# Optimization experiments

Hardware: AMD Instinct MI355X
Metric: run time of the kernel (lower is better)

## Reference

```python
import jax, jax.numpy as jnp
import numpy as np

N = 50000      # nodes
E = 1600000    # message edges (avg degree 32)
EQ = 500000    # link-prediction query edges
IN, HID, OUT, FCH = 128, 128, 64, 256
ALPHA = 0.5


def setup_inputs() -> dict:
    key = jax.random.key(0)
    ks = jax.random.split(key, 8)
    def p(k, shape):
        fan_in = shape[0]
        return jax.random.normal(k, shape, jnp.float32) * (1.0 / np.sqrt(fan_in))
    return {
        "x": jax.random.normal(ks[0], (N, IN), jnp.float32),
        "edge_index": jax.random.randint(ks[1], (2, E), 0, N),
        "edge_label_index": jax.random.randint(ks[2], (2, EQ), 0, N),
        "W1": p(ks[3], (IN, HID)),  "b1": jnp.zeros((HID,), jnp.float32),
        "W2": p(ks[4], (HID, OUT)), "b2": jnp.zeros((OUT,), jnp.float32),
        "Wf1": p(ks[5], (IN, FCH)), "bf1": jnp.zeros((FCH,), jnp.float32),
        "Wf2": p(ks[6], (FCH, OUT)), "bf2": jnp.zeros((OUT,), jnp.float32),
    }


def reference(x, edge_index, edge_label_index, W1, b1, W2, b2, Wf1, bf1, Wf2, bf2):
    n = x.shape[0]
    # GCN self-loops + symmetric normalization (PyG GCNConv defaults)
    loop = jnp.arange(n)
    src = jnp.concatenate([edge_index[0], loop])
    dst = jnp.concatenate([edge_index[1], loop])
    deg = jax.ops.segment_sum(jnp.ones_like(dst, jnp.float32), dst, num_segments=n)
    dinv = jnp.where(deg > 0, jax.lax.rsqrt(deg), 0.0)
    norm = dinv[src] * dinv[dst]  # [E+N]

    def gcn(h, W, b):
        h = h @ W                                  # transform first (PyG order)
        msg = norm[:, None] * h[src]               # gather + scale per edge
        return jax.ops.segment_sum(msg, dst, num_segments=n) + b

    x_gcn = jax.nn.relu(gcn(x, W1, b1))
    x_gcn = gcn(x_gcn, W2, b2)
    x_fc = jax.nn.relu(x @ Wf1 + bf1) @ Wf2 + bf2
    z = x_gcn * (1.0 - ALPHA) + x_fc * ALPHA       # [N, OUT]
    # edge dot-product decode
    return jnp.sum(z[edge_label_index[0]] * z[edge_label_index[1]], axis=1)
```

## Files before the change

### kernel.cpp

```cpp
#include <hip/hip_runtime.h>

#define FIN   128
#define FHID  128
#define FOUT  64
#define FFC   256
#define CHUNK 4096
#define BKBITS 7
#define BKN   128
#define ECAP  4608

typedef __attribute__((ext_vector_type(8))) short          bf16x8;
typedef __attribute__((ext_vector_type(4))) float          f32x4;
typedef __attribute__((ext_vector_type(2))) float          f32x2;
typedef __attribute__((ext_vector_type(8))) unsigned short u16x8;

static __device__ __forceinline__ unsigned short f2bf(float f) {
    unsigned int u = __float_as_uint(f);
    u = (u + 0x7fffu + ((u >> 16) & 1u)) >> 16;
    return (unsigned short)u;
}
static __device__ __forceinline__ float bf2f(unsigned short s) {
    return __uint_as_float(((unsigned int)s) << 16);
}
static __device__ __forceinline__ void accum_fp8(float* acc, uint4 g) {
    f32x2 p;
    p = __builtin_amdgcn_cvt_pk_f32_fp8(g.x, false); acc[0]  += p.x; acc[1]  += p.y;
    p = __builtin_amdgcn_cvt_pk_f32_fp8(g.x, true);  acc[2]  += p.x; acc[3]  += p.y;
    p = __builtin_amdgcn_cvt_pk_f32_fp8(g.y, false); acc[4]  += p.x; acc[5]  += p.y;
    p = __builtin_amdgcn_cvt_pk_f32_fp8(g.y, true);  acc[6]  += p.x; acc[7]  += p.y;
    p = __builtin_amdgcn_cvt_pk_f32_fp8(g.z, false); acc[8]  += p.x; acc[9]  += p.y;
    p = __builtin_amdgcn_cvt_pk_f32_fp8(g.z, true);  acc[10] += p.x; acc[11] += p.y;
    p = __builtin_amdgcn_cvt_pk_f32_fp8(g.w, false); acc[12] += p.x; acc[13] += p.y;
    p = __builtin_amdgcn_cvt_pk_f32_fp8(g.w, true);  acc[14] += p.x; acc[15] += p.y;
}

__global__ __launch_bounds__(256) void cvt_kernel(
    const float* __restrict__ W1, const float* __restrict__ W2,
    const float* __restrict__ Wf1, const float* __restrict__ Wf2,
    unsigned short* __restrict__ w1t, unsigned short* __restrict__ w2t,
    unsigned short* __restrict__ wf1t, unsigned short* __restrict__ wf2t)
{
    long i = (long)blockIdx.x * 256 + threadIdx.x;
    if (i < 16384) {
        int k = (int)i >> 7, n = (int)i & 127;
        w1t[n * 128 + k] = f2bf(W1[i]);
    } else if (i < 24576) {
        int j = (int)i - 16384; int k = j >> 6, n = j & 63;
        w2t[n * 128 + k] = f2bf(W2[j]);
    } else if (i < 57344) {
        int j = (int)i - 24576; int k = j >> 8, n = j & 255;
        wf1t[n * 128 + k] = f2bf(Wf1[j]);
    } else if (i < 73728) {
        int j = (int)i - 57344; int k = j >> 6, n = j & 63;
        wf2t[n * 256 + k] = f2bf(Wf2[j]);
    }
}

__global__ __launch_bounds__(256) void binA_fc_kernel(
    const int* __restrict__ src, const int* __restrict__ dst,
    int* __restrict__ bcur, unsigned int* __restrict__ ebuf, int E, int NBA,
    const float* __restrict__ X,
    const unsigned short* __restrict__ B1T,
    const unsigned short* __restrict__ B2T,
    const float* __restrict__ bias1, const float* __restrict__ bias2,
    unsigned short* __restrict__ C, int M)
{
    __shared__ __align__(16) unsigned char smem[49152];
    const int tid = threadIdx.x;

    if (blockIdx.x < NBA) {
        int* hist   = (int*)smem;
        int* rstart = (int*)(smem + 2048);
        int* lcur   = (int*)(smem + 4096);
        int t = tid;
        hist[t] = 0; hist[t + 256] = 0; lcur[t] = 0; lcur[t + 256] = 0;
        __syncthreads();
        int e0 = blockIdx.x * CHUNK;
        int cnt_e = min(CHUNK, E - e0);
        int sreg[16], dreg[16];
        #pragma unroll
        for (int i = 0; i < 16; i++) {
            int o = t + i * 256;
            bool ok = o < cnt_e;
            sreg[i] = ok ? src[e0 + o] : 0;
            dreg[i] = ok ? dst[e0 + o] : 0;
            if (ok) ;
        }
        #pragma unroll
        for (int i = 0; i < 16; i++)
            if (t + i * 256 < cnt_e) atomicAdd(&hist[dreg[i] >> BKBITS], 1);
        __syncthreads();
        if (hist[t])       rstart[t]       = atomicAdd(&bcur[t],       hist[t]);
        if (hist[t + 256]) rstart[t + 256] = atomicAdd(&bcur[t + 256], hist[t + 256]);
        __syncthreads();
        #pragma unroll
        for (int i = 0; i < 16; i++) {
            if (t + i * 256 < cnt_e) {
                int s = sreg[i], d = dreg[i];
                int b = d >> BKBITS;
                int pos = rstart[b] + atomicAdd(&lcur[b], 1);
                if (pos < ECAP)
                    ebuf[(size_t)b * ECAP + pos] =
                        ((unsigned)s << BKBITS) | ((unsigned)d & (BKN - 1));
            }
        }
        return;
    }

    unsigned short* lds = (unsigned short*)smem;
    const int lane = tid & 63;
    const int wave = tid >> 6;
    const int m = lane & 15;
    const int q = lane >> 4;
    const int rowbase = (blockIdx.x - NBA) * 64 + wave * 16;
    const int row = rowbase + m;

    float4 av[8] = {};
    {
        const float* arow = X + (size_t)row * FIN + q * 8;
        if (row < M) {
            #pragma unroll
            for (int kk = 0; kk < 4; kk++) {
                av[2 * kk]     = *(const float4*)(arow + kk * 32);
                av[2 * kk + 1] = *(const float4*)(arow + kk * 32 + 4);
            }
        }
    }

    #pragma unroll 2
    for (int i = tid; i < 2048; i += 256) {
        int n = i >> 4, sl = i & 15;
        ((u16x8*)lds)[(n << 4) | (sl ^ (n & 7))] = ((const u16x8*)B1T)[i];
    }
    __syncthreads();

    f32x4 acc[16] = {};
    for (int k0 = 0; k0 < 128; k0 += 32) {
        int kk = k0 >> 5;
        float4 a0 = av[2 * kk], a1 = av[2 * kk + 1];
        bf16x8 a;
        a[0] = (short)f2bf(a0.x); a[1] = (short)f2bf(a0.y);
        a[2] = (short)f2bf(a0.z); a[3] = (short)f2bf(a0.w);
        a[4] = (short)f2bf(a1.x); a[5] = (short)f2bf(a1.y);
        a[6] = (short)f2bf(a1.z); a[7] = (short)f2bf(a1.w);
        int sl = q + (k0 >> 3);
        #pragma unroll
        for (int c = 0; c < 8; c++) {
            int cc = c * 16 + m;
            bf16x8 b = ((const bf16x8*)lds)[(cc << 4) | (sl ^ (cc & 7))];
            acc[c] = __builtin_amdgcn_mfma_f32_16x16x32_bf16(a, b, acc[c], 0, 0, 0);
        }
    }
    __syncthreads();
    #pragma unroll 2
    for (int i = tid; i < 2048; i += 256) {
        int n = i >> 4, sl = i & 15;
        ((u16x8*)lds)[(n << 4) | (sl ^ (n & 7))] = ((const u16x8*)B1T)[2048 + i];
    }
    __syncthreads();
    for (int k0 = 0; k0 < 128; k0 += 32) {
        int kk = k0 >> 5;
        float4 a0 = av[2 * kk], a1 = av[2 * kk + 1];
        bf16x8 a;
        a[0] = (short)f2bf(a0.x); a[1] = (short)f2bf(a0.y);
        a[2] = (short)f2bf(a0.z); a[3] = (short)f2bf(a0.w);
        a[4] = (short)f2bf(a1.x); a[5] = (short)f2bf(a1.y);
        a[6] = (short)f2bf(a1.z); a[7] = (short)f2bf(a1.w);
        int sl = q + (k0 >> 3);
        #pragma unroll
        for (int c = 0; c < 8; c++) {
            int cc = c * 16 + m;
            bf16x8 b = ((const bf16x8*)lds)[(cc << 4) | (sl ^ (cc & 7))];
            acc[8 + c] = __builtin_amdgcn_mfma_f32_16x16x32_bf16(a, b, acc[8 + c], 0, 0, 0);
        }
    }
    __syncthreads();
    #pragma unroll
    for (int c = 0; c < 16; c++) {
        int cc = c * 16 + m;
        float bv = bias1[cc];
        #pragma unroll
        for (int r = 0; r < 4; r++) {
            int rr = wave * 16 + q * 4 + r;
            float v = fmaxf(acc[c][r] + bv, 0.f);
            lds[rr * 256 + ((((cc >> 3) ^ (rr & 7)) << 3) | (cc & 7))] = f2bf(v);
        }
    }
    for (int i = tid; i < 1024; i += 256) {
        int n = i >> 4, sl = i & 15;
        ((u16x8*)lds)[2048 + ((n << 4) | (sl ^ (n & 7)))] =
            ((const u16x8*)B2T)[n * 32 + sl];
    }
    __syncthreads();

    f32x4 acc2[4] = {};
    {
        int rr = wave * 16 + m;
        for (int k0 = 0; k0 < 128; k0 += 32) {
            int sl = q + (k0 >> 3);
            bf16x8 a = ((const bf16x8*)lds)[(rr << 5) | (sl ^ (rr & 7))];
            #pragma unroll
            for (int c = 0; c < 4; c++) {
                int cc = c * 16 + m;
                bf16x8 b = ((const bf16x8*)lds)[2048 + ((cc << 4) | (sl ^ (cc & 7)))];
                acc2[c] = __builtin_amdgcn_mfma_f32_16x16x32_bf16(a, b, acc2[c], 0, 0, 0);
            }
        }
    }
    __syncthreads();
    for (int i = tid; i < 1024; i += 256) {
        int n = i >> 4, sl = i & 15;
        ((u16x8*)lds)[2048 + ((n << 4) | (sl ^ (n & 7)))] =
            ((const u16x8*)B2T)[n * 32 + 16 + sl];
    }
    __syncthreads();
    {
        int rr = wave * 16 + m;
        for (int k0 = 128; k0 < 256; k0 += 32) {
            int sla = q + (k0 >> 3);
            int slb = q + ((k0 - 128) >> 3);
            bf16x8 a = ((const bf16x8*)lds)[(rr << 5) | (sla ^ (rr & 7))];
            #pragma unroll
            for (int c = 0; c < 4; c++) {
                int cc = c * 16 + m;
                bf16x8 b = ((const bf16x8*)lds)[2048 + ((cc << 4) | (slb ^ (cc & 7)))];
                acc2[c] = __builtin_amdgcn_mfma_f32_16x16x32_bf16(a, b, acc2[c], 0, 0, 0);
            }
        }
    }
    __syncthreads();

    constexpr int ROWB = 4 * 16 * 2 + 16;
    unsigned char* wbase = (unsigned char*)lds + wave * 16 * ROWB;
    #pragma unroll
    for (int c = 0; c < 4; c++) {
        int lc = c * 16 + m;
        float bv = bias2[lc];
        #pragma unroll
        for (int r = 0; r < 4; r++)
            ((unsigned short*)(wbase + (q * 4 + r) * ROWB))[lc] =
                f2bf(acc2[c][r] + bv);
    }
    #pragma unroll
    for (int p = 0; p < 2; p++) {
        int r2 = p * 8 + (lane >> 3);
        int bo = (lane & 7) * 16;
        int gr = rowbase + r2;
        if (gr < M) {
            uint4 v = *(const uint4*)(wbase + r2 * ROWB + bo);
            *(uint4*)((unsigned char*)C + (size_t)gr * FOUT * 2 + bo) = v;
        }
    }
}

__global__ __launch_bounds__(256) void binB_kernel(
    const unsigned int* __restrict__ ebuf, const int* __restrict__ bcnt,
    int2* __restrict__ rp2, int* __restrict__ col, float* __restrict__ dinv,
    const float* __restrict__ x, unsigned char* __restrict__ xs, int N)
{
    __shared__ __align__(16) unsigned char smem[40448];
    int* cnt           = (int*)smem;
    int* tmp           = (int*)(smem + 512);
    int* ccur          = (int*)(smem + 1536);
    int* scur          = (int*)(smem + 2048);
    float* sdinv       = (float*)(smem + 3072);
    unsigned int* skey = (unsigned int*)(smem + 3584);
    int* colLds        = (int*)(smem + 22016);
    int b = blockIdx.x;
    int t = threadIdx.x;
    size_t base = (size_t)b * ECAP;
    int ne = min(bcnt[b], ECAP);
    if (t < 128) cnt[t] = 0;
    scur[t] = 0;
    __syncthreads();
    for (int e = t; e < ne; e += 256) {
        unsigned int k = ebuf[base + e];
        atomicAdd(&cnt[k & (BKN - 1)], 1);
        atomicAdd(&scur[k >> 15], 1);
    }
    __syncthreads();
    int c = (t < 128) ? cnt[t] : 0;
    tmp[t] = c;
    __syncthreads();
    int acc = c;
    for (int off = 1; off < 128; off <<= 1) {
        int a = (t >= off) ? tmp[t - off] : 0;
        __syncthreads();
        acc += a; tmp[t] = acc;
        __syncthreads();
    }
    if (t < 128) {
        float di = rsqrtf((float)c + 1.0f);
        sdinv[t] = di;
        int node = b * BKN + t;
        int st = (int)base + acc - c;
        if (node < N) { dinv[node] = di; rp2[node] = make_int2(st, st + c); }
        ccur[t] = acc - c;
    }
    __syncthreads();
    int sv = scur[t];
    tmp[t] = sv;
    __syncthreads();
    int sacc = sv;
    for (int off = 1; off < 256; off <<= 1) {
        int a = (t >= off) ? tmp[t - off] : 0;
        __syncthreads();
        sacc += a; tmp[t] = sacc;
        __syncthreads();
    }
    scur[t] = sacc - sv;
    __syncthreads();
    for (int e = t; e < ne; e += 256) {
        unsigned int k = ebuf[base + e];
        int pos = atomicAdd(&scur[k >> 15], 1);
        skey[pos] = k;
    }
    __syncthreads();
    for (int w = 0; w < ne; w += 256) {
        int e = w + t;
        if (e < ne) {
            unsigned int k = skey[e];
            int pos = atomicAdd(&ccur[k & (BKN - 1)], 1);
            colLds[pos] = (int)(k >> BKBITS);
        }
        __syncthreads();
    }
    for (int e = t; e < ne; e += 256)
        col[base + e] = colLds[e];
    int nl0 = t >> 3;
    int f0 = (t & 7) << 4;
    #pragma unroll
    for (int it = 0; it < 4; it++) {
        int nl = it * 32 + nl0;
        int gn = b * BKN + nl;
        if (gn >= N) continue;
        float d2 = sdinv[nl];
        const float* xr = x + (size_t)gn * FIN + f0;
        float4 va = *(const float4*)(xr);
        float4 vb = *(const float4*)(xr + 4);
        float4 vc = *(const float4*)(xr + 8);
        float4 vd = *(const float4*)(xr + 12);
        float f[16] = { va.x * d2, va.y * d2, va.z * d2, va.w * d2,
                        vb.x * d2, vb.y * d2, vb.z * d2, vb.w * d2,
                        vc.x * d2, vc.y * d2, vc.z * d2, vc.w * d2,
                        vd.x * d2, vd.y * d2, vd.z * d2, vd.w * d2 };
        uint4 w;
        w.x = 0; w.y = 0; w.z = 0; w.w = 0;
        w.x = __builtin_amdgcn_cvt_pk_fp8_f32(f[0],  f[1],  w.x, false);
        w.x = __builtin_amdgcn_cvt_pk_fp8_f32(f[2],  f[3],  w.x, true);
        w.y = __builtin_amdgcn_cvt_pk_fp8_f32(f[4],  f[5],  w.y, false);
        w.y = __builtin_amdgcn_cvt_pk_fp8_f32(f[6],  f[7],  w.y, true);
        w.z = __builtin_amdgcn_cvt_pk_fp8_f32(f[8],  f[9],  w.z, false);
        w.z = __builtin_amdgcn_cvt_pk_fp8_f32(f[10], f[11], w.z, true);
        w.w = __builtin_amdgcn_cvt_pk_fp8_f32(f[12], f[13], w.w, false);
        w.w = __builtin_amdgcn_cvt_pk_fp8_f32(f[14], f[15], w.w, true);
        *(uint4*)(xs + (size_t)gn * 128 + f0) = w;
    }
}

__global__ __launch_bounds__(256) void pull1_kernel(
    const unsigned char* __restrict__ xs, const int2* __restrict__ rp2,
    const int* __restrict__ col, const float* __restrict__ dinv,
    unsigned short* __restrict__ aggx, int N)
{
    int tid = threadIdx.x;
    int node = blockIdx.x * 32 + (tid >> 3);
    if (node >= N) return;
    int f0 = (tid & 7) << 4;
    const unsigned char* base = xs + f0;
    float di = dinv[node];
    int2 se = rp2[node];
    float acc[16] = {};
    accum_fp8(acc, *(const uint4*)(base + (size_t)node * 128));
    int e = se.x, end = se.y;
    for (; e + 4 <= end; e += 4) {
        int s0 = col[e], s1 = col[e + 1], s2 = col[e + 2], s3 = col[e + 3];
        uint4 g0 = *(const uint4*)(base + (size_t)s0 * 128);
        uint4 g1 = *(const uint4*)(base + (size_t)s1 * 128);
        uint4 g2 = *(const uint4*)(base + (size_t)s2 * 128);
        uint4 g3 = *(const uint4*)(base + (size_t)s3 * 128);
        accum_fp8(acc, g0); accum_fp8(acc, g1);
        accum_fp8(acc, g2); accum_fp8(acc, g3);
    }
    for (; e < end; e++)
        accum_fp8(acc, *(const uint4*)(base + (size_t)col[e] * 128));
    u16x8 o0, o1;
    #pragma unroll
    for (int j = 0; j < 8; j++) {
        o0[j] = f2bf(di * acc[j]);
        o1[j] = f2bf(di * acc[8 + j]);
    }
    *(u16x8*)(aggx + (size_t)node * FIN + f0)     = o0;
    *(u16x8*)(aggx + (size_t)node * FIN + f0 + 8) = o1;
}

__global__ __launch_bounds__(256) void gcn_kernel(
    const unsigned short* __restrict__ A,
    const unsigned short* __restrict__ B1T,
    const unsigned short* __restrict__ B2T,
    const float* __restrict__ bias1,
    const float* __restrict__ rowscale,
    unsigned short* __restrict__ C, int M)
{
    __shared__ __align__(16) unsigned short lds[16384];
    const int tid  = threadIdx.x;
    const int lane = tid & 63;
    const int wave = tid >> 6;
    const int m = lane & 15;
    const int q = lane >> 4;
    const int rowbase = blockIdx.x * 64 + wave * 16;
    const int row = rowbase + m;

    bf16x8 areg[4] = {};
    {
        const unsigned short* arow = A + (size_t)row * FIN + q * 8;
        if (row < M) {
            #pragma unroll
            for (int kk = 0; kk < 4; kk++)
                areg[kk] = *(const bf16x8*)(arow + kk * 32);
        }
    }

    #pragma unroll 2
    for (int i = tid; i < 2048; i += 256) {
        int n = i >> 4, sl = i & 15;
        ((u16x8*)lds)[(n << 4) | (sl ^ (n & 7))] = ((const u16x8*)B1T)[i];
    }
    __syncthreads();

    f32x4 acc[8] = {};
    for (int k0 = 0; k0 < 128; k0 += 32) {
        bf16x8 a = areg[k0 >> 5];
        int sl = q + (k0 >> 3);
        #pragma unroll
        for (int c = 0; c < 8; c++) {
            int cc = c * 16 + m;
            bf16x8 b = ((const bf16x8*)lds)[(cc << 4) | (sl ^ (cc & 7))];
            acc[c] = __builtin_amdgcn_mfma_f32_16x16x32_bf16(a, b, acc[c], 0, 0, 0);
        }
    }
    __syncthreads();

    #pragma unroll
    for (int c = 0; c < 8; c++) {
        int cc = c * 16 + m;
        float bv = bias1[cc];
        #pragma unroll
        for (int r = 0; r < 4; r++) {
            int rr = wave * 16 + q * 4 + r;
            float v = fmaxf(acc[c][r] + bv, 0.f);
            lds[rr * 128 + ((((cc >> 3) ^ (rr & 7)) << 3) | (cc & 7))] = f2bf(v);
        }
    }
    for (int i = tid; i < 1024; i += 256) {
        int n = i >> 4, sl = i & 15;
        ((u16x8*)lds)[1024 + ((n << 4) | (sl ^ (n & 7)))] = ((const u16x8*)B2T)[i];
    }
    __syncthreads();

    f32x4 acc2[4] = {};
    {
        int rr = wave * 16 + m;
        for (int k0 = 0; k0 < 128; k0 += 32) {
            int sl = q + (k0 >> 3);
            bf16x8 a = ((const bf16x8*)lds)[(rr << 4) | (sl ^ (rr & 7))];
            #pragma unroll
            for (int c = 0; c < 4; c++) {
                int cc = c * 16 + m;
                bf16x8 b = ((const bf16x8*)lds)[1024 + ((cc << 4) | (sl ^ (cc & 7)))];
                acc2[c] = __builtin_amdgcn_mfma_f32_16x16x32_bf16(a, b, acc2[c], 0, 0, 0);
            }
        }
    }
    float rs[4];
    #pragma unroll
    for (int r = 0; r < 4; r++) {
        int gr = rowbase + q * 4 + r;
        rs[r] = (gr < M) ? rowscale[gr] : 1.0f;
    }
    __syncthreads();

    constexpr int ROWB = 4 * 16 * 2 + 16;
    unsigned char* wbase = (unsigned char*)lds + wave * 16 * ROWB;
    #pragma unroll
    for (int c = 0; c < 4; c++) {
        int lc = c * 16 + m;
        #pragma unroll
        for (int r = 0; r < 4; r++)
            ((unsigned short*)(wbase + (q * 4 + r) * ROWB))[lc] =
                f2bf(acc2[c][r] * rs[r]);
    }
    #pragma unroll
    for (int p = 0; p < 2; p++) {
        int r2 = p * 8 + (lane >> 3);
        int bo = (lane & 7) * 16;
        int gr = rowbase + r2;
        if (gr < M) {
            uint4 v = *(const uint4*)(wbase + r2 * ROWB + bo);
            *(uint4*)((unsigned char*)C + (size_t)gr * FOUT * 2 + bo) = v;
        }
    }
}

__global__ __launch_bounds__(256) void pull2_kernel(
    const unsigned short* __restrict__ t2s, const int2* __restrict__ rp2,
    const int* __restrict__ col, const float* __restrict__ dinv,
    const unsigned short* __restrict__ xfc, const float* __restrict__ b2,
    unsigned short* __restrict__ zbf, int N)
{
    int tid = threadIdx.x;
    int node = blockIdx.x * 32 + (tid >> 3);
    if (node >= N) return;
    int f0 = (tid & 7) << 3;
    const unsigned short* base = t2s + f0;
    float di = dinv[node];
    u16x8 xv = *(const u16x8*)(xfc + (size_t)node * FOUT + f0);
    float4 bb0 = *(const float4*)(b2 + f0);
    float4 bb1 = *(const float4*)(b2 + f0 + 4);
    u16x8 own = *(const u16x8*)(base + (size_t)node * FOUT);
    float acc[8];
    #pragma unroll
    for (int j = 0; j < 8; j++) acc[j] = bf2f(own[j]);
    int2 se = rp2[node];
    int e = se.x, end = se.y;
    for (; e + 4 <= end; e += 4) {
        int s0 = col[e], s1 = col[e + 1], s2 = col[e + 2], s3 = col[e + 3];
        u16x8 v0 = *(const u16x8*)(base + (size_t)s0 * FOUT);
        u16x8 v1 = *(const u16x8*)(base + (size_t)s1 * FOUT);
        u16x8 v2 = *(const u16x8*)(base + (size_t)s2 * FOUT);
        u16x8 v3 = *(const u16x8*)(base + (size_t)s3 * FOUT);
        #pragma unroll
        for (int j = 0; j < 8; j++)
            acc[j] += (bf2f(v0[j]) + bf2f(v1[j])) + (bf2f(v2[j]) + bf2f(v3[j]));
    }
    for (; e < end; e++) {
        u16x8 v = *(const u16x8*)(base + (size_t)col[e] * FOUT);
        #pragma unroll
        for (int j = 0; j < 8; j++) acc[j] += bf2f(v[j]);
    }
    float bv[8] = { bb0.x, bb0.y, bb0.z, bb0.w, bb1.x, bb1.y, bb1.z, bb1.w };
    u16x8 o;
    #pragma unroll
    for (int j = 0; j < 8; j++)
        o[j] = f2bf(0.5f * (di * acc[j] + bv[j]) + 0.5f * bf2f(xv[j]));
    *(u16x8*)(zbf + (size_t)node * FOUT + f0) = o;
}

__global__ void decode_kernel(
    const unsigned short* __restrict__ zbf, const int* __restrict__ eli,
    float* __restrict__ out, int Q)
{
    int tid = blockIdx.x * blockDim.x + threadIdx.x;
    int q = tid >> 3;
    if (q >= Q) return;
    int lane = tid & 7;
    int a = eli[q];
    int b = eli[Q + q];
    u16x8 va = *(const u16x8*)(zbf + (size_t)a * FOUT + lane * 8);
    u16x8 vb = *(const u16x8*)(zbf + (size_t)b * FOUT + lane * 8);
    float s = 0.f;
    #pragma unroll
    for (int j = 0; j < 8; j++) s += bf2f(va[j]) * bf2f(vb[j]);
    s += __shfl_down(s, 4, 8);
    s += __shfl_down(s, 2, 8);
    s += __shfl_down(s, 1, 8);
    if (lane == 0) out[q] = s;
}

extern "C" void kernel_launch(void* const* d_in, const int* in_sizes, int n_in,
                              void* d_out, int out_size, void* d_ws, size_t ws_size,
                              hipStream_t stream)
{
    const float* x   = (const float*)d_in[0];
    const int*   ei  = (const int*)  d_in[1];
    const int*   eli = (const int*)  d_in[2];
    const float* W1  = (const float*)d_in[3];
    const float* b1  = (const float*)d_in[4];
    const float* W2  = (const float*)d_in[5];
    const float* b2  = (const float*)d_in[6];
    const float* Wf1 = (const float*)d_in[7];
    const float* bf1 = (const float*)d_in[8];
    const float* Wf2 = (const float*)d_in[9];
    const float* bf2 = (const float*)d_in[10];
    float* out = (float*)d_out;

    const int N = in_sizes[0] / FIN;
    const int E = in_sizes[1] / 2;
    const int Q = in_sizes[2] / 2;
    const int* src = ei;
    const int* dst = ei + E;
    const int NBK = (N + BKN - 1) >> BKBITS;
    const int NBA = (E + CHUNK - 1) / CHUNK;
    const int NCV = 73728 / 256;
    const int NFC = (N + 63) / 64;

    char* p = (char*)d_ws;
    float* dinv = (float*)p;             p += (size_t)N * 4;
    int2*  rp2  = (int2*)p;              p += (size_t)N * 8;
    int*   bcur = (int*)p;               p += 2048;
    unsigned short* w1t  = (unsigned short*)p; p += FIN * FHID * 2;
    unsigned short* w2t  = (unsigned short*)p; p += FHID * FOUT * 2;
    unsigned short* wf1t = (unsigned short*)p; p += FIN * FFC * 2;
    unsigned short* wf2t = (unsigned short*)p; p += FFC * FOUT * 2;
    unsigned short* xfc = (unsigned short*)p;  p += (size_t)N * FOUT * 2;
    unsigned char* xs = (unsigned char*)p;     p += (size_t)N * 128;
    unsigned int* ebuf = (unsigned int*)p;  p += (size_t)NBK * ECAP * 4;
    int*   col  = (int*)p;               p += (size_t)NBK * ECAP * 4;
    unsigned short* aggx = (unsigned short*)p; p += (size_t)N * FIN * 2;
    unsigned short* t2s  = (unsigned short*)p; p += (size_t)N * FOUT * 2;
    unsigned short* zbf  = (unsigned short*)p; p += (size_t)N * FOUT * 2;

    const int TB = 256;

    hipMemsetAsync(bcur, 0, 2048, stream);

    cvt_kernel<<<NCV, TB, 0, stream>>>(
        W1, W2, Wf1, Wf2, w1t, w2t, wf1t, wf2t);

    binA_fc_kernel<<<NBA + NFC, TB, 0, stream>>>(
        src, dst, bcur, ebuf, E, NBA,
        x, wf1t, wf2t, bf1, bf2, xfc, N);

    binB_kernel<<<NBK, TB, 0, stream>>>(ebuf, bcur, rp2, col, dinv, x, xs, N);

    pull1_kernel<<<(N + 31) / 32, TB, 0, stream>>>(xs, rp2, col, dinv, aggx, N);

    gcn_kernel<<<(N + 63) / 64, TB, 0, stream>>>(
        aggx, w1t, w2t, b1, dinv, t2s, N);

    pull2_kernel<<<(N + 31) / 32, TB, 0, stream>>>(
        t2s, rp2, col, dinv, xfc, b2, zbf, N);

    {
        long total = (long)Q * 8;
        decode_kernel<<<(int)((total + TB - 1) / TB), TB, 0, stream>>>(
            zbf, eli, out, Q);
    }
}
```

Baseline: 236.8 us.

## Locally sort binning chunk in LDS for coalesced bucket writes; cache ebuf in LDS

The edge-binning blocks now run a block-wide prefix scan over the per-bucket histogram and scatter keys into an LDS staging array ordered by bucket. They then write each bucket's run contiguously to global memory, replacing scattered per-edge global stores. The CSR-build kernel loads its bucket's ebuf slice into LDS once and reuses it for both passes instead of reading global memory twice. The cost is extra scan loops and __syncthreads in the binning phase, and the bucket index is packed into the high key bits, which assumes node ids fit in 16 bits.

```diff
diff --git a/kernel.cpp b/kernel.cpp
--- a/kernel.cpp
+++ b/kernel.cpp
@@ -70,8 +70,10 @@
 
     if (blockIdx.x < NBA) {
         int* hist   = (int*)smem;
-        int* rstart = (int*)(smem + 2048);
-        int* lcur   = (int*)(smem + 4096);
+        int* lstart = (int*)(smem + 2048);
+        int* rstart = (int*)(smem + 4096);
+        int* lcur   = (int*)(smem + 6144);
+        unsigned int* skey = (unsigned int*)(smem + 8192);
         int t = tid;
         hist[t] = 0; hist[t + 256] = 0; lcur[t] = 0; lcur[t + 256] = 0;
         __syncthreads();
@@ -84,24 +86,57 @@
             bool ok = o < cnt_e;
             sreg[i] = ok ? src[e0 + o] : 0;
             dreg[i] = ok ? dst[e0 + o] : 0;
-            if (ok) ;
         }
         #pragma unroll
         for (int i = 0; i < 16; i++)
             if (t + i * 256 < cnt_e) atomicAdd(&hist[dreg[i] >> BKBITS], 1);
         __syncthreads();
-        if (hist[t])       rstart[t]       = atomicAdd(&bcur[t],       hist[t]);
-        if (hist[t + 256]) rstart[t + 256] = atomicAdd(&bcur[t + 256], hist[t + 256]);
+        int v0 = hist[t];
+        lstart[t] = v0;
+        __syncthreads();
+        int a0 = v0;
+        for (int off = 1; off < 256; off <<= 1) {
+            int xv = (t >= off) ? lstart[t - off] : 0;
+            __syncthreads();
+            a0 += xv; lstart[t] = a0;
+            __syncthreads();
+        }
+        int carry = lstart[255];
+        int v1 = hist[t + 256];
+        rstart[t] = v1;
+        __syncthreads();
+        int a1 = v1;
+        for (int off = 1; off < 256; off <<= 1) {
+            int xv = (t >= off) ? rstart[t - off] : 0;
+            __syncthreads();
+            a1 += xv; rstart[t] = a1;
+            __syncthreads();
+        }
+        lstart[t] = a0 - v0;
+        lstart[t + 256] = carry + a1 - v1;
+        __syncthreads();
+        if (v0) rstart[t]       = atomicAdd(&bcur[t],       v0);
+        if (v1) rstart[t + 256] = atomicAdd(&bcur[t + 256], v1);
         __syncthreads();
         #pragma unroll
         for (int i = 0; i < 16; i++) {
             if (t + i * 256 < cnt_e) {
-                int s = sreg[i], d = dreg[i];
-                int b = d >> BKBITS;
-                int pos = rstart[b] + atomicAdd(&lcur[b], 1);
-                if (pos < ECAP)
-                    ebuf[(size_t)b * ECAP + pos] =
-                        ((unsigned)s << BKBITS) | ((unsigned)d & (BKN - 1));
+                int b = dreg[i] >> BKBITS;
+                int pos = lstart[b] + atomicAdd(&lcur[b], 1);
+                skey[pos] = ((unsigned)b << 23) | ((unsigned)sreg[i] << BKBITS)
+                          | ((unsigned)dreg[i] & (BKN - 1));
+            }
+        }
+        __syncthreads();
+        #pragma unroll
+        for (int i = 0; i < 16; i++) {
+            int e = t + i * 256;
+            if (e < cnt_e) {
+                unsigned int k = skey[e];
+                int b = (int)(k >> 23);
+                int gpos = rstart[b] + (e - lstart[b]);
+                if (gpos < ECAP)
+                    ebuf[(size_t)b * ECAP + gpos] = k & 0x7FFFFFu;
             }
         }
         return;
@@ -273,8 +308,11 @@
     if (t < 128) cnt[t] = 0;
     scur[t] = 0;
     __syncthreads();
+    for (int e = t; e < ne; e += 256)
+        colLds[e] = (int)ebuf[base + e];
+    __syncthreads();
     for (int e = t; e < ne; e += 256) {
-        unsigned int k = ebuf[base + e];
+        unsigned int k = (unsigned int)colLds[e];
         atomicAdd(&cnt[k & (BKN - 1)], 1);
         atomicAdd(&scur[k >> 15], 1);
     }
@@ -311,7 +349,7 @@
     scur[t] = sacc - sv;
     __syncthreads();
     for (int e = t; e < ne; e += 256) {
-        unsigned int k = ebuf[base + e];
+        unsigned int k = (unsigned int)colLds[e];
         int pos = atomicAdd(&scur[k >> 15], 1);
         skey[pos] = k;
     }
```

New measurement: 233.7 us. About the same (-1.3%).
